# Performance work log

Measured on AMD Instinct MI355X. Metric: run time of the kernel, lower is better.

The kernel has to match this reference:

```python
import jax, jax.numpy as jnp
import numpy as np

N = 100000   # nodes
E = 1600000  # edges
DF = 256     # dim_features
H = 64       # hidden (layers=[64,64])
T = 4        # dim_target
G = 8        # graphs in batch
BN_EPS = 1e-5


def setup_inputs() -> dict:
    key = jax.random.key(0)
    ks = jax.random.split(key, 16)
    x = jax.random.normal(ks[0], (N, DF), jnp.float32)
    edge_index = jax.random.randint(ks[1], (2, E), 0, N)
    batch = jnp.sort(jax.random.randint(ks[2], (N,), 0, G))

    def lin(k, fan_in, fan_out):
        return jax.random.normal(k, (fan_in, fan_out), jnp.float32) / np.sqrt(fan_in)

    return {
        "x": x,
        "edge_index": edge_index,
        "batch": batch,
        # first_h: Linear(DF,H)+BN+ReLU
        "W_first": lin(ks[3], DF, H),
        "b_first": jnp.zeros((H,), jnp.float32),
        "bn1_g": jnp.ones((H,), jnp.float32),
        "bn1_b": jnp.zeros((H,), jnp.float32),
        # linears[0]: Linear(H,T)
        "W_lin0": lin(ks[4], H, T),
        "b_lin0": jnp.zeros((T,), jnp.float32),
        # GINConv nn: Linear(H,H)+BN+ReLU
        "W_conv": lin(ks[5], H, H),
        "b_conv": jnp.zeros((H,), jnp.float32),
        "bn2_g": jnp.ones((H,), jnp.float32),
        "bn2_b": jnp.zeros((H,), jnp.float32),
        # linears[1]: Linear(H,T)
        "W_lin1": lin(ks[6], H, T),
        "b_lin1": jnp.zeros((T,), jnp.float32),
    }


def _bn(h, gamma, beta):
    # BatchNorm1d in training mode: batch statistics over node dim
    mu = h.mean(axis=0)
    var = h.var(axis=0)
    return gamma * (h - mu) / jnp.sqrt(var + BN_EPS) + beta


def reference(x, edge_index, batch,
              W_first, b_first, bn1_g, bn1_b,
              W_lin0, b_lin0,
              W_conv, b_conv, bn2_g, bn2_b,
              W_lin1, b_lin1):
    # Layer 0: first_h = Linear+BN+ReLU
    f = jax.nn.relu(_bn(x @ W_first + b_first, bn1_g, bn1_b))  # [N,H]
    np0 = f @ W_lin0 + b_lin0                                  # [N,T]
    node_pred = np0
    wsi_pred = jax.ops.segment_max(np0, batch, num_segments=G)  # global_max_pool

    # Layer 1: GINConv (eps=0): nn(x_i + sum_{j->i} x_j)
    src, dst = edge_index[0], edge_index[1]
    agg = jax.ops.segment_sum(f[src], dst, num_segments=N)     # [N,H]
    h = f + agg
    f = jax.nn.relu(_bn(h @ W_conv + b_conv, bn2_g, bn2_b))    # [N,H]
    np1 = f @ W_lin1 + b_lin1                                  # [N,T]
    node_pred = node_pred + np1
    wsi_pred = wsi_pred + jax.ops.segment_max(np1, batch, num_segments=G)

    return wsi_pred, node_pred
```

## Files before the change

### kernel.cpp

```cpp
#include <hip/hip_runtime.h>
#include <math.h>

#define NN 100000
#define NE 1600000
#define DF 256
#define HH 64
#define TT 4
#define GG 8
#define BN_EPS 1e-5f
#define NTOT (NE + NN)

#define BROWS 512
#define NBK ((NN + BROWS - 1) / BROWS)
#define BCAP 10240
#define PCHUNK 1600
#define NPB (NE / PCHUNK)

typedef __attribute__((ext_vector_type(8))) short short8v;
typedef __attribute__((ext_vector_type(4))) float f32x4;
typedef unsigned short ushort_t;
typedef unsigned int uint_t;

__device__ __forceinline__ void atomicMaxF(float* addr, float val) {
  if (val >= 0.f) atomicMax((int*)addr, __float_as_int(val));
  else            atomicMin((unsigned int*)addr, __float_as_uint(val));
}

__device__ __forceinline__ short f2bf(float f) {
  uint_t u = __float_as_uint(f);
  u += 0x7FFFu + ((u >> 16) & 1u);
  return (short)(u >> 16);
}
__device__ __forceinline__ float bf2f(uint_t u) { return __uint_as_float(u << 16); }
__device__ __forceinline__ float bfhi(uint_t u) { return __uint_as_float(u & 0xFFFF0000u); }

__global__ void k_setup(const float* __restrict__ Wf, const float* __restrict__ Wc,
                        const float* __restrict__ Wl0,
                        short8v* __restrict__ Wpk, short8v* __restrict__ Wpk2,
                        short8v* __restrict__ hpk,
                        float* __restrict__ stats, float* __restrict__ maxb,
                        int* __restrict__ Bcnt) {
  int i = blockIdx.x * 256 + threadIdx.x;
  if (i < 2048) {
    int fi = i >> 6, le = i & 63;
    int s = fi >> 2, ct = fi & 3, li = le & 15, lh = le >> 4;
    short8v v;
#pragma unroll
    for (int e = 0; e < 8; ++e)
      v[e] = f2bf(Wf[(32 * s + 8 * lh + e) * HH + ct * 16 + li]);
    Wpk[i] = v;
  } else if (i < 2560) {
    int j = i - 2048;
    int fi = j >> 6, le = j & 63;
    int s = fi >> 2, ct = fi & 3, li = le & 15, lh = le >> 4;
    short8v v;
#pragma unroll
    for (int e = 0; e < 8; ++e)
      v[e] = f2bf(Wc[(32 * s + 8 * lh + e) * HH + ct * 16 + li]);
    Wpk2[j] = v;
  } else if (i < 2688) {
    int j = i - 2560;
    int s = j >> 6, le = j & 63;
    int li = le & 15, lh = le >> 4;
    short8v v;
#pragma unroll
    for (int e = 0; e < 8; ++e)
      v[e] = (li < TT) ? f2bf(Wl0[(32 * s + 8 * lh + e) * TT + li]) : (short)0;
    hpk[j] = v;
  }
  if (i < 512) stats[i] = 0.f;
  if (i < 64)  maxb[i]  = -INFINITY;
  if (i < NBK) Bcnt[i]  = 0;
}

__global__ __launch_bounds__(256, 2) void k_gemm1_mfma(
    const float* __restrict__ x, const short8v* __restrict__ Wpk,
    const float* __restrict__ b, ushort_t* __restrict__ h1,
    float* __restrict__ stats) {
  const int lane = threadIdx.x & 63;
  const int li = lane & 15;
  const int lh = lane >> 4;
  const int gw = (blockIdx.x * 256 + (int)threadIdx.x) >> 6;
  const int nw = (gridDim.x * 256) >> 6;

  short8v bf[8][4];
#pragma unroll
  for (int s = 0; s < 8; ++s)
#pragma unroll
    for (int ct = 0; ct < 4; ++ct)
      bf[s][ct] = Wpk[(s * 4 + ct) * 64 + lane];

  float bias[4];
#pragma unroll
  for (int ct = 0; ct < 4; ++ct) bias[ct] = b[ct * 16 + li];

  float ps[4] = {0.f, 0.f, 0.f, 0.f}, pss[4] = {0.f, 0.f, 0.f, 0.f};

  for (int t = gw; t < NN / 16; t += nw) {
    const float* xb = x + (size_t)(t * 16 + li) * DF + 8 * lh;
    f32x4 acc[4];
#pragma unroll
    for (int ct = 0; ct < 4; ++ct) acc[ct] = (f32x4){0.f, 0.f, 0.f, 0.f};

#pragma unroll
    for (int s = 0; s < 8; ++s) {
      float4 a0 = *(const float4*)(xb + 32 * s);
      float4 a1 = *(const float4*)(xb + 32 * s + 4);
      short8v af;
      af[0] = f2bf(a0.x); af[1] = f2bf(a0.y); af[2] = f2bf(a0.z); af[3] = f2bf(a0.w);
      af[4] = f2bf(a1.x); af[5] = f2bf(a1.y); af[6] = f2bf(a1.z); af[7] = f2bf(a1.w);
#pragma unroll
      for (int ct = 0; ct < 4; ++ct)
        acc[ct] = __builtin_amdgcn_mfma_f32_16x16x32_bf16(af, bf[s][ct], acc[ct], 0, 0, 0);
    }

    ushort_t* hb = h1 + (size_t)t * 16 * HH;
#pragma unroll
    for (int ct = 0; ct < 4; ++ct) {
#pragma unroll
      for (int r = 0; r < 4; ++r) {
        float h = acc[ct][r] + bias[ct];
        hb[(lh * 4 + r) * HH + ct * 16 + li] = (ushort_t)f2bf(h);
        ps[ct] += h; pss[ct] += h * h;
      }
    }
  }

#pragma unroll
  for (int ct = 0; ct < 4; ++ct) {
    ps[ct]  += __shfl_xor(ps[ct], 16);  ps[ct]  += __shfl_xor(ps[ct], 32);
    pss[ct] += __shfl_xor(pss[ct], 16); pss[ct] += __shfl_xor(pss[ct], 32);
  }
  if (lane < 16) {
#pragma unroll
    for (int ct = 0; ct < 4; ++ct) {
      atomicAdd(&stats[ct * 16 + lane], ps[ct]);
      atomicAdd(&stats[HH + ct * 16 + lane], pss[ct]);
    }
  }
}

__global__ __launch_bounds__(256) void k_norm_gemm2(
    const ushort_t* __restrict__ h1, const float* __restrict__ stats,
    const float* __restrict__ gamma, const float* __restrict__ beta,
    const short8v* __restrict__ Wpk2, const short8v* __restrict__ hpk,
    const float* __restrict__ bl0,
    const int* __restrict__ batch,
    float* __restrict__ node_pred, float* __restrict__ maxbuf,
    ushort_t* __restrict__ g) {
  __shared__ float lmax[GG * TT];
  __shared__ float abl[128];
  if (threadIdx.x < GG * TT) lmax[threadIdx.x] = -INFINITY;
  if (threadIdx.x < 64) {
    int c = threadIdx.x;
    float mu  = stats[c] * (1.f / NN);
    float var = stats[HH + c] * (1.f / NN) - mu * mu;
    float a = gamma[c] * rsqrtf(var + BN_EPS);
    abl[c] = a;
    abl[HH + c] = beta[c] - mu * a;
  }
  __syncthreads();

  const int lane = threadIdx.x & 63;
  const int li = lane & 15;
  const int lh = lane >> 4;
  const int gw = (blockIdx.x * 256 + (int)threadIdx.x) >> 6;
  const int nw = (gridDim.x * 256) >> 6;

  short8v bfr[2][4];
#pragma unroll
  for (int s = 0; s < 2; ++s)
#pragma unroll
    for (int ct = 0; ct < 4; ++ct)
      bfr[s][ct] = Wpk2[(s * 4 + ct) * 64 + lane];

  short8v bhd[2];
#pragma unroll
  for (int s = 0; s < 2; ++s)
    bhd[s] = hpk[s * 64 + lane];

  const float4 sa0 = *(const float4*)(abl + 8 * lh);
  const float4 sa1 = *(const float4*)(abl + 8 * lh + 4);
  const float4 sb0 = *(const float4*)(abl + HH + 8 * lh);
  const float4 sb1 = *(const float4*)(abl + HH + 8 * lh + 4);
  const float4 ta0 = *(const float4*)(abl + 32 + 8 * lh);
  const float4 ta1 = *(const float4*)(abl + 32 + 8 * lh + 4);
  const float4 tb0 = *(const float4*)(abl + HH + 32 + 8 * lh);
  const float4 tb1 = *(const float4*)(abl + HH + 32 + 8 * lh + 4);
  const float blv = (li < TT) ? bl0[li] : 0.f;

  for (int t = gw; t < NN / 16; t += nw) {
    const ushort_t* hb = h1 + (size_t)(t * 16 + li) * HH + 8 * lh;
    uint4 xa = *(const uint4*)(hb);
    uint4 xc = *(const uint4*)(hb + 32);

    short8v af0, af1;
    af0[0] = f2bf(fmaxf(fmaf(sa0.x, bf2f(xa.x), sb0.x), 0.f));
    af0[1] = f2bf(fmaxf(fmaf(sa0.y, bfhi(xa.x), sb0.y), 0.f));
    af0[2] = f2bf(fmaxf(fmaf(sa0.z, bf2f(xa.y), sb0.z), 0.f));
    af0[3] = f2bf(fmaxf(fmaf(sa0.w, bfhi(xa.y), sb0.w), 0.f));
    af0[4] = f2bf(fmaxf(fmaf(sa1.x, bf2f(xa.z), sb1.x), 0.f));
    af0[5] = f2bf(fmaxf(fmaf(sa1.y, bfhi(xa.z), sb1.y), 0.f));
    af0[6] = f2bf(fmaxf(fmaf(sa1.z, bf2f(xa.w), sb1.z), 0.f));
    af0[7] = f2bf(fmaxf(fmaf(sa1.w, bfhi(xa.w), sb1.w), 0.f));
    af1[0] = f2bf(fmaxf(fmaf(ta0.x, bf2f(xc.x), tb0.x), 0.f));
    af1[1] = f2bf(fmaxf(fmaf(ta0.y, bfhi(xc.x), tb0.y), 0.f));
    af1[2] = f2bf(fmaxf(fmaf(ta0.z, bf2f(xc.y), tb0.z), 0.f));
    af1[3] = f2bf(fmaxf(fmaf(ta0.w, bfhi(xc.y), tb0.w), 0.f));
    af1[4] = f2bf(fmaxf(fmaf(ta1.x, bf2f(xc.z), tb1.x), 0.f));
    af1[5] = f2bf(fmaxf(fmaf(ta1.y, bfhi(xc.z), tb1.y), 0.f));
    af1[6] = f2bf(fmaxf(fmaf(ta1.z, bf2f(xc.w), tb1.z), 0.f));
    af1[7] = f2bf(fmaxf(fmaf(ta1.w, bfhi(xc.w), tb1.w), 0.f));

    f32x4 acc[4], acch;
#pragma unroll
    for (int ct = 0; ct < 4; ++ct) {
      acc[ct] = (f32x4){0.f, 0.f, 0.f, 0.f};
      acc[ct] = __builtin_amdgcn_mfma_f32_16x16x32_bf16(af0, bfr[0][ct], acc[ct], 0, 0, 0);
      acc[ct] = __builtin_amdgcn_mfma_f32_16x16x32_bf16(af1, bfr[1][ct], acc[ct], 0, 0, 0);
    }
    acch = (f32x4){0.f, 0.f, 0.f, 0.f};
    acch = __builtin_amdgcn_mfma_f32_16x16x32_bf16(af0, bhd[0], acch, 0, 0, 0);
    acch = __builtin_amdgcn_mfma_f32_16x16x32_bf16(af1, bhd[1], acch, 0, 0, 0);

    ushort_t* gb = g + (size_t)t * 16 * HH;
#pragma unroll
    for (int ct = 0; ct < 4; ++ct)
#pragma unroll
      for (int r = 0; r < 4; ++r)
        gb[(lh * 4 + r) * HH + ct * 16 + li] = (ushort_t)f2bf(acc[ct][r]);

    if (li < TT) {
#pragma unroll
      for (int r = 0; r < 4; ++r) {
        int row = t * 16 + lh * 4 + r;
        float np = acch[r] + blv;
        atomicMaxF(&lmax[batch[row] * TT + li], np);
        node_pred[(size_t)row * TT + li] = np;
      }
    }
  }
  __syncthreads();
  if (threadIdx.x < GG * TT) atomicMaxF(&maxbuf[threadIdx.x], lmax[threadIdx.x]);
}

__global__ __launch_bounds__(256) void k_norm_np(
    const ushort_t* __restrict__ hin, const float* __restrict__ stats,
    const float* __restrict__ gamma, const float* __restrict__ beta,
    const float* __restrict__ Wlin, const float* __restrict__ blin,
    const int* __restrict__ batch, float* __restrict__ node_pred,
    float* __restrict__ maxbuf, int rpb) {
  __shared__ float lmax[GG * TT];
  __shared__ float abl[128];
  if (threadIdx.x < GG * TT) lmax[threadIdx.x] = -INFINITY;
  if (threadIdx.x < 64) {
    int c = threadIdx.x;
    float mu  = stats[c] * (1.f / NN);
    float var = stats[HH + c] * (1.f / NN) - mu * mu;
    float a = gamma[c] * rsqrtf(var + BN_EPS);
    abl[c] = a;
    abl[HH + c] = beta[c] - mu * a;
  }
  __syncthreads();

  const int lane = threadIdx.x & 63;
  const int wid  = threadIdx.x >> 6;
  const float a  = abl[lane];
  const float b2 = abl[HH + lane];
  const float4 w = ((const float4*)Wlin)[lane];
  const float4 bl = *(const float4*)blin;
  int r0 = blockIdx.x * rpb;
  int r1 = min(r0 + rpb, NN);

  for (int r = r0 + wid; r < r1; r += 4) {
    float h = bf2f(hin[(size_t)r * HH + lane]);
    float f = fmaxf(fmaf(a, h, b2), 0.f);
    float p0 = f * w.x, p1 = f * w.y, p2 = f * w.z, p3 = f * w.w;
#pragma unroll
    for (int off = 32; off; off >>= 1) {
      p0 += __shfl_xor(p0, off);
      p1 += __shfl_xor(p1, off);
      p2 += __shfl_xor(p2, off);
      p3 += __shfl_xor(p3, off);
    }
    if (lane == 0) {
      float4 np;
      np.x = p0 + bl.x; np.y = p1 + bl.y; np.z = p2 + bl.z; np.w = p3 + bl.w;
      int g = batch[r];
      atomicMaxF(&lmax[g * TT + 0], np.x);
      atomicMaxF(&lmax[g * TT + 1], np.y);
      atomicMaxF(&lmax[g * TT + 2], np.z);
      atomicMaxF(&lmax[g * TT + 3], np.w);
      float4* op = (float4*)(node_pred + (size_t)r * TT);
      float4 o = *op;
      np.x += o.x; np.y += o.y; np.z += o.z; np.w += o.w;
      *op = np;
    }
  }
  __syncthreads();
  if (threadIdx.x < GG * TT) atomicMaxF(&maxbuf[threadIdx.x], lmax[threadIdx.x]);
}

__global__ __launch_bounds__(256) void k_part(
    const int* __restrict__ ei, int* __restrict__ Bcnt,
    uint2* __restrict__ ebuf) {
  __shared__ int hist[256], start[256], cnt[256], gbase[256];
  __shared__ int ssrc[PCHUNK], sdst[PCHUNK];
  const int t = threadIdx.x;
  hist[t] = 0; cnt[t] = 0;
  __syncthreads();
  const int e0 = blockIdx.x * PCHUNK;
  for (int i = t; i < PCHUNK; i += 256)
    atomicAdd(&hist[ei[NE + e0 + i] >> 9], 1);
  __syncthreads();
  int v = hist[t];
  start[t] = v;
  __syncthreads();
  for (int off = 1; off < 256; off <<= 1) {
    int u = (t >= off) ? start[t - off] : 0;
    __syncthreads();
    start[t] += u;
    __syncthreads();
  }
  int incl = start[t];
  __syncthreads();
  start[t] = incl - v;
  if (v > 0) gbase[t] = atomicAdd(&Bcnt[t], v);
  __syncthreads();
  for (int i = t; i < PCHUNK; i += 256) {
    int src = ei[e0 + i];
    int dst = ei[NE + e0 + i];
    int b = dst >> 9;
    int p = start[b] + atomicAdd(&cnt[b], 1);
    ssrc[p] = src; sdst[p] = dst;
  }
  __syncthreads();
  for (int i = t; i < PCHUNK; i += 256) {
    int dst = sdst[i];
    int b = dst >> 9;
    uint2 pr; pr.x = (uint_t)ssrc[i]; pr.y = (uint_t)dst;
    ebuf[(size_t)b * BCAP + gbase[b] + (i - start[b])] = pr;
  }
}

__global__ void k_bscan(const int* __restrict__ Bcnt, int* __restrict__ Bbase) {
  __shared__ int s[256];
  int t = threadIdx.x;
  int v = 0;
  if (t < NBK) {
    int rows = min(BROWS, NN - t * BROWS);
    v = Bcnt[t] + rows;
  }
  s[t] = v;
  __syncthreads();
  for (int off = 1; off < 256; off <<= 1) {
    int u = (t >= off) ? s[t - off] : 0;
    __syncthreads();
    s[t] += u;
    __syncthreads();
  }
  if (t < NBK) Bbase[t] = s[t] - v;
}

__global__ __launch_bounds__(256) void k_fill2(
    const int* __restrict__ Bcnt, const int* __restrict__ Bbase,
    const uint2* __restrict__ ebuf, int* __restrict__ rowstart,
    int* __restrict__ srcl) {
  __shared__ int cnt[BROWS];
  __shared__ int ssum[256];
  const int b = blockIdx.x;
  const int r0 = b * BROWS;
  const int nrows = min(BROWS, NN - r0);
  const int ne = Bcnt[b];
  const int base = Bbase[b];
  const uint2* eb = ebuf + (size_t)b * BCAP;
  const int t = threadIdx.x;

  cnt[2 * t] = (2 * t < nrows) ? 1 : 0;
  cnt[2 * t + 1] = (2 * t + 1 < nrows) ? 1 : 0;
  __syncthreads();
  for (int j = t; j < ne; j += 256)
    atomicAdd(&cnt[(int)eb[j].y - r0], 1);
  __syncthreads();

  int a0 = cnt[2 * t], a1 = cnt[2 * t + 1];
  ssum[t] = a0 + a1;
  __syncthreads();
  for (int off = 1; off < 256; off <<= 1) {
    int u = (t >= off) ? ssum[t - off] : 0;
    __syncthreads();
    ssum[t] += u;
    __syncthreads();
  }
  int e0 = base + ssum[t] - (a0 + a1);
  int e1 = e0 + a0;
  __syncthreads();
  if (2 * t < nrows)     { rowstart[r0 + 2 * t] = e0;     srcl[e0] = r0 + 2 * t; }
  if (2 * t + 1 < nrows) { rowstart[r0 + 2 * t + 1] = e1; srcl[e1] = r0 + 2 * t + 1; }
  cnt[2 * t] = e0 + 1;
  cnt[2 * t + 1] = e1 + 1;
  __syncthreads();
  for (int j = t; j < ne; j += 256) {
    uint2 pr = eb[j];
    int p = atomicAdd(&cnt[(int)pr.y - r0], 1);
    srcl[p] = (int)pr.x;
  }
}

#define RF(x) __builtin_amdgcn_readfirstlane(x)
#define GLD(V, I) asm volatile("global_load_ushort %0, %1, %2" \
    : "=v"(V) : "v"(voff), "s"(g + (size_t)(I) * HH) : "memory")
#define WAIT16 do { asm volatile("s_waitcnt vmcnt(16)" ::: "memory"); \
    __builtin_amdgcn_sched_barrier(0); } while (0)
#define WAIT0 do { asm volatile("s_waitcnt vmcnt(0)" ::: "memory"); \
    __builtin_amdgcn_sched_barrier(0); } while (0)
#define ISSUE16(P, EB) do { \
  int j0 = RF(srcl[(EB) + 0]),  j1 = RF(srcl[(EB) + 1]); \
  int j2 = RF(srcl[(EB) + 2]),  j3 = RF(srcl[(EB) + 3]); \
  int j4 = RF(srcl[(EB) + 4]),  j5 = RF(srcl[(EB) + 5]); \
  int j6 = RF(srcl[(EB) + 6]),  j7 = RF(srcl[(EB) + 7]); \
  int j8 = RF(srcl[(EB) + 8]),  j9 = RF(srcl[(EB) + 9]); \
  int j10 = RF(srcl[(EB) + 10]), j11 = RF(srcl[(EB) + 11]); \
  int j12 = RF(srcl[(EB) + 12]), j13 = RF(srcl[(EB) + 13]); \
  int j14 = RF(srcl[(EB) + 14]), j15 = RF(srcl[(EB) + 15]); \
  GLD(P##0, j0);  GLD(P##1, j1);  GLD(P##2, j2);  GLD(P##3, j3); \
  GLD(P##4, j4);  GLD(P##5, j5);  GLD(P##6, j6);  GLD(P##7, j7); \
  GLD(P##8, j8);  GLD(P##9, j9);  GLD(P##10, j10); GLD(P##11, j11); \
  GLD(P##12, j12); GLD(P##13, j13); GLD(P##14, j14); GLD(P##15, j15); \
} while (0)
#define CJ(V, EI) do { \
  if ((EI) == nb) { \
    h2[(size_t)cur * HH + lane] = (ushort_t)f2bf(acc); ps += acc; pss += acc * acc; \
    cur++; nb = __builtin_amdgcn_readlane(rsv, cur - wra); acc = bc; \
  } \
  acc += bf2f(V); } while (0)
#define CONS16(P, EB) do { \
  CJ(P##0, (EB) + 0);  CJ(P##1, (EB) + 1);  CJ(P##2, (EB) + 2);  CJ(P##3, (EB) + 3); \
  CJ(P##4, (EB) + 4);  CJ(P##5, (EB) + 5);  CJ(P##6, (EB) + 6);  CJ(P##7, (EB) + 7); \
  CJ(P##8, (EB) + 8);  CJ(P##9, (EB) + 9);  CJ(P##10, (EB) + 10); CJ(P##11, (EB) + 11); \
  CJ(P##12, (EB) + 12); CJ(P##13, (EB) + 13); CJ(P##14, (EB) + 14); CJ(P##15, (EB) + 15); \
} while (0)

__global__ __launch_bounds__(256) void k_gather(
    const ushort_t* __restrict__ g, const int* __restrict__ rowstart,
    const int* __restrict__ srcl, const float* __restrict__ bias,
    ushort_t* __restrict__ h2, float* __restrict__ stats) {
  const int lane = threadIdx.x & 63;
  const int wid  = threadIdx.x >> 6;
  const float bc = bias[lane];
  const uint_t voff = lane * 2;
  const int wra = (blockIdx.x * 4 + wid) * 8;

  int ridx = wra + 1 + lane;
  int rsv = (ridx < NN) ? rowstart[ridx] : NTOT;

  int e    = RF(rowstart[wra]);
  int eEnd = __builtin_amdgcn_readlane(rsv, 7);
  int cur  = wra;
  int nb   = __builtin_amdgcn_readlane(rsv, 0);
  float acc = bc, ps = 0.f, pss = 0.f;

  uint_t A0, A1, A2, A3, A4, A5, A6, A7, A8, A9, A10, A11, A12, A13, A14, A15;
  uint_t B0, B1, B2, B3, B4, B5, B6, B7, B8, B9, B10, B11, B12, B13, B14, B15;

  int n = (eEnd - e) >> 4;
  if (n > 0) {
    int pend = e;
    ISSUE16(A, e); e += 16; n--;
    while (n >= 2) {
      int eb = e;
      ISSUE16(B, e); e += 16; n--;
      WAIT16; CONS16(A, pend); pend = eb;
      int ea = e;
      ISSUE16(A, e); e += 16; n--;
      WAIT16; CONS16(B, pend); pend = ea;
    }
    if (n == 1) {
      int eb = e;
      ISSUE16(B, e); e += 16;
      WAIT16; CONS16(A, pend); pend = eb;
      WAIT0;  CONS16(B, pend);
    } else {
      WAIT0;  CONS16(A, pend);
    }
  }
  for (; e < eEnd; ++e) {
    if (e == nb) {
      h2[(size_t)cur * HH + lane] = (ushort_t)f2bf(acc); ps += acc; pss += acc * acc;
      cur++; nb = __builtin_amdgcn_readlane(rsv, cur - wra); acc = bc;
    }
    int i = RF(srcl[e]);
    acc += bf2f(g[(size_t)i * HH + lane]);
  }
  h2[(size_t)cur * HH + lane] = (ushort_t)f2bf(acc); ps += acc; pss += acc * acc;

  __shared__ float sred[4][128];
  sred[wid][lane] = ps;
  sred[wid][64 + lane] = pss;
  __syncthreads();
  if (wid == 0) {
    float s0 = sred[0][lane] + sred[1][lane] + sred[2][lane] + sred[3][lane];
    float q0 = sred[0][64 + lane] + sred[1][64 + lane] + sred[2][64 + lane] + sred[3][64 + lane];
    atomicAdd(&stats[lane], s0);
    atomicAdd(&stats[HH + lane], q0);
  }
}

__global__ void k_wsi(const float* __restrict__ m0, const float* __restrict__ m1,
                      float* __restrict__ out) {
  int i = threadIdx.x;
  out[i] = m0[i] + m1[i];
}

extern "C" void kernel_launch(void* const* d_in, const int* in_sizes, int n_in,
                              void* d_out, int out_size, void* d_ws, size_t ws_size,
                              hipStream_t stream) {
  const float* x    = (const float*)d_in[0];
  const int*   ei   = (const int*)d_in[1];
  const int*   bat  = (const int*)d_in[2];
  const float* Wf   = (const float*)d_in[3];
  const float* bf   = (const float*)d_in[4];
  const float* g1   = (const float*)d_in[5];
  const float* be1  = (const float*)d_in[6];
  const float* Wl0  = (const float*)d_in[7];
  const float* bl0  = (const float*)d_in[8];
  const float* Wc   = (const float*)d_in[9];
  const float* bc   = (const float*)d_in[10];
  const float* g2   = (const float*)d_in[11];
  const float* be2  = (const float*)d_in[12];
  const float* Wl1  = (const float*)d_in[13];
  const float* bl1  = (const float*)d_in[14];

  float* out   = (float*)d_out;
  float* wsi   = out;
  float* npred = out + GG * TT;

  ushort_t* h2bf   = (ushort_t*)d_ws;
  ushort_t* h1bf   = h2bf + (size_t)NN * HH;
  ushort_t* gbf    = h1bf + (size_t)NN * HH;
  float*    stats1 = (float*)(gbf + (size_t)NN * HH);
  float*    stats2 = stats1 + 256;
  float*    maxb   = stats2 + 256;
  int*      rowstart = (int*)(maxb + 64);
  int*      Bcnt     = rowstart + NN;
  int*      Bbase    = Bcnt + 256;
  int*      srcl     = Bbase + 256;
  uint2*    ebuf     = (uint2*)(srcl + NTOT);
  short8v*  Wpk      = (short8v*)(ebuf + (size_t)NBK * BCAP);
  short8v*  Wpk2     = Wpk + 2048;
  short8v*  hpk      = Wpk2 + 512;

  k_setup<<<dim3(11), dim3(256), 0, stream>>>(Wf, Wc, Wl0, Wpk, Wpk2, hpk,
                                              stats1, maxb, Bcnt);
  k_part<<<dim3(NPB), dim3(256), 0, stream>>>(ei, Bcnt, ebuf);
  k_bscan<<<dim3(1), dim3(256), 0, stream>>>(Bcnt, Bbase);
  k_fill2<<<dim3(NBK), dim3(256), 0, stream>>>(Bcnt, Bbase, ebuf, rowstart, srcl);

  k_gemm1_mfma<<<dim3(512), dim3(256), 0, stream>>>(x, Wpk, bf, h1bf, stats1);
  k_norm_gemm2<<<dim3(512), dim3(256), 0, stream>>>(
      h1bf, stats1, g1, be1, Wpk2, hpk, bl0, bat, npred, maxb, gbf);

  k_gather<<<dim3(NN / 32), dim3(256), 0, stream>>>(
      gbf, rowstart, srcl, bc, h2bf, stats2);
  k_norm_np<<<dim3(512), dim3(256), 0, stream>>>(
      h2bf, stats2, g2, be2, Wl1, bl1, bat, npred, maxb + 32, (NN + 511) / 512);

  k_wsi<<<dim3(1), dim3(32), 0, stream>>>(maxb, maxb + 32, wsi);
}
```

Baseline: 293.5 us.

## Split GEMM1 K dimension across wave pairs with LDS partial-sum exchange

```diff
diff --git a/kernel.cpp b/kernel.cpp
--- a/kernel.cpp
+++ b/kernel.cpp
@@ -9,6 +9,8 @@
 #define GG 8
 #define BN_EPS 1e-5f
 #define NTOT (NE + NN)
+#define NTILE (NN / 16)
+#define NPAIRS 1024
 
 #define BROWS 512
 #define NBK ((NN + BROWS - 1) / BROWS)
@@ -73,69 +75,87 @@
   if (i < NBK) Bcnt[i]  = 0;
 }
 
-__global__ __launch_bounds__(256, 2) void k_gemm1_mfma(
+__global__ __launch_bounds__(256, 3) void k_gemm1_mfma(
     const float* __restrict__ x, const short8v* __restrict__ Wpk,
     const float* __restrict__ b, ushort_t* __restrict__ h1,
     float* __restrict__ stats) {
+  __shared__ float ex[2][2][64][8];
   const int lane = threadIdx.x & 63;
+  const int wid  = threadIdx.x >> 6;
+  const int p    = wid >> 1;
+  const int kh   = wid & 1;
   const int li = lane & 15;
   const int lh = lane >> 4;
-  const int gw = (blockIdx.x * 256 + (int)threadIdx.x) >> 6;
-  const int nw = (gridDim.x * 256) >> 6;
-
-  short8v bf[8][4];
-#pragma unroll
-  for (int s = 0; s < 8; ++s)
+
+  short8v bf[4][4];
+#pragma unroll
+  for (int ss = 0; ss < 4; ++ss)
 #pragma unroll
     for (int ct = 0; ct < 4; ++ct)
-      bf[s][ct] = Wpk[(s * 4 + ct) * 64 + lane];
-
-  float bias[4];
-#pragma unroll
-  for (int ct = 0; ct < 4; ++ct) bias[ct] = b[ct * 16 + li];
-
-  float ps[4] = {0.f, 0.f, 0.f, 0.f}, pss[4] = {0.f, 0.f, 0.f, 0.f};
-
-  for (int t = gw; t < NN / 16; t += nw) {
-    const float* xb = x + (size_t)(t * 16 + li) * DF + 8 * lh;
+      bf[ss][ct] = Wpk[((4 * kh + ss) * 4 + ct) * 64 + lane];
+
+  float bias[2];
+#pragma unroll
+  for (int j = 0; j < 2; ++j) bias[j] = b[(2 * kh + j) * 16 + li];
+
+  float ps[2] = {0.f, 0.f}, pss[2] = {0.f, 0.f};
+
+  const int t0 = blockIdx.x * 2 + p;
+  const int nt = (NTILE + NPAIRS - 1) / NPAIRS;
+  for (int it = 0; it < nt; ++it) {
+    int t = t0 + it * NPAIRS;
+    bool act = t < NTILE;
     f32x4 acc[4];
 #pragma unroll
     for (int ct = 0; ct < 4; ++ct) acc[ct] = (f32x4){0.f, 0.f, 0.f, 0.f};
 
-#pragma unroll
-    for (int s = 0; s < 8; ++s) {
-      float4 a0 = *(const float4*)(xb + 32 * s);
-      float4 a1 = *(const float4*)(xb + 32 * s + 4);
-      short8v af;
-      af[0] = f2bf(a0.x); af[1] = f2bf(a0.y); af[2] = f2bf(a0.z); af[3] = f2bf(a0.w);
-      af[4] = f2bf(a1.x); af[5] = f2bf(a1.y); af[6] = f2bf(a1.z); af[7] = f2bf(a1.w);
-#pragma unroll
-      for (int ct = 0; ct < 4; ++ct)
-        acc[ct] = __builtin_amdgcn_mfma_f32_16x16x32_bf16(af, bf[s][ct], acc[ct], 0, 0, 0);
-    }
-
-    ushort_t* hb = h1 + (size_t)t * 16 * HH;
-#pragma unroll
-    for (int ct = 0; ct < 4; ++ct) {
-#pragma unroll
-      for (int r = 0; r < 4; ++r) {
-        float h = acc[ct][r] + bias[ct];
-        hb[(lh * 4 + r) * HH + ct * 16 + li] = (ushort_t)f2bf(h);
-        ps[ct] += h; pss[ct] += h * h;
+    if (act) {
+      const float* xb = x + (size_t)(t * 16 + li) * DF + 128 * kh + 8 * lh;
+#pragma unroll
+      for (int ss = 0; ss < 4; ++ss) {
+        float4 a0 = *(const float4*)(xb + 32 * ss);
+        float4 a1 = *(const float4*)(xb + 32 * ss + 4);
+        short8v af;
+        af[0] = f2bf(a0.x); af[1] = f2bf(a0.y); af[2] = f2bf(a0.z); af[3] = f2bf(a0.w);
+        af[4] = f2bf(a1.x); af[5] = f2bf(a1.y); af[6] = f2bf(a1.z); af[7] = f2bf(a1.w);
+#pragma unroll
+        for (int ct = 0; ct < 4; ++ct)
+          acc[ct] = __builtin_amdgcn_mfma_f32_16x16x32_bf16(af, bf[ss][ct], acc[ct], 0, 0, 0);
       }
-    }
-  }
-
-#pragma unroll
-  for (int ct = 0; ct < 4; ++ct) {
-    ps[ct]  += __shfl_xor(ps[ct], 16);  ps[ct]  += __shfl_xor(ps[ct], 32);
-    pss[ct] += __shfl_xor(pss[ct], 16); pss[ct] += __shfl_xor(pss[ct], 32);
+      int oc = 2 * (1 - kh);
+#pragma unroll
+      for (int j = 0; j < 2; ++j)
+#pragma unroll
+        for (int r = 0; r < 4; ++r)
+          ex[p][kh][lane][4 * j + r] = acc[oc + j][r];
+    }
+    __syncthreads();
+    if (act) {
+      ushort_t* hb = h1 + (size_t)t * 16 * HH;
+#pragma unroll
+      for (int j = 0; j < 2; ++j) {
+        int ct = 2 * kh + j;
+#pragma unroll
+        for (int r = 0; r < 4; ++r) {
+          float h = acc[ct][r] + ex[p][1 - kh][lane][4 * j + r] + bias[j];
+          hb[(lh * 4 + r) * HH + ct * 16 + li] = (ushort_t)f2bf(h);
+          ps[j] += h; pss[j] += h * h;
+        }
+      }
+    }
+    __syncthreads();
+  }
+
+#pragma unroll
+  for (int j = 0; j < 2; ++j) {
+    ps[j]  += __shfl_xor(ps[j], 16);  ps[j]  += __shfl_xor(ps[j], 32);
+    pss[j] += __shfl_xor(pss[j], 16); pss[j] += __shfl_xor(pss[j], 32);
   }
   if (lane < 16) {
 #pragma unroll
-    for (int ct = 0; ct < 4; ++ct) {
-      atomicAdd(&stats[ct * 16 + lane], ps[ct]);
-      atomicAdd(&stats[HH + ct * 16 + lane], pss[ct]);
+    for (int j = 0; j < 2; ++j) {
+      atomicAdd(&stats[(2 * kh + j) * 16 + lane], ps[j]);
+      atomicAdd(&stats[HH + (2 * kh + j) * 16 + lane], pss[j]);
     }
   }
 }
```

Measured after the change: 277.0 us. 1.06x faster.
